# Optimization experiments

Measured on AMD Instinct MI355X. Metric: run time of the kernel, lower is better.

The kernel has to match this reference:

```python
import jax, jax.numpy as jnp
import numpy as np

N = 8192
IN_F = 256
OUT_F = 256
ATTN_DIM = 2
NEG_INF = -1e18


def setup_inputs() -> dict:
    key = jax.random.key(0)
    k1, k2, k3, k4, k5 = jax.random.split(key, 5)
    node_feats = jax.random.normal(k1, (N, IN_F), dtype=jnp.float32)
    Ahat = (jax.random.uniform(k2, (N, N)) < 0.01).astype(jnp.float32)
    # ensure no isolated rows (self loops) so softmax rows are well-defined
    Ahat = Ahat.at[jnp.arange(N), jnp.arange(N)].set(1.0)
    bound_w = 1.0 / np.sqrt(IN_F)
    bound_wa = 1.0 / np.sqrt(OUT_F)
    bound_a = 1.0 / np.sqrt(2 * ATTN_DIM)
    w = jax.random.uniform(k3, (IN_F, OUT_F), minval=-bound_w, maxval=bound_w, dtype=jnp.float32)
    w_a = jax.random.uniform(k4, (OUT_F, ATTN_DIM), minval=-bound_wa, maxval=bound_wa, dtype=jnp.float32)
    a = jax.random.uniform(k5, (2 * ATTN_DIM, 1), minval=-bound_a, maxval=bound_a, dtype=jnp.float32)
    return {"node_feats": node_feats, "Ahat": Ahat, "w": w, "w_a": w_a, "a": a}


def reference(node_feats, Ahat, w, w_a, a):
    # h_prime: [N, out_features]
    h_prime = node_feats @ w
    # h_reduced: [N, attn_dim]
    h_reduced = h_prime @ w_a
    # e[i, j] = cat(h_red[i], h_red[j]) @ a  ==  h_red[i]@a[:d] + h_red[j]@a[d:]
    # (identical math to the repeat+cat+matmul in the original, without the
    #  O(N^2 * 2d) materialization)
    f_src = (h_reduced @ a[:ATTN_DIM]).squeeze(-1)  # [N]
    f_dst = (h_reduced @ a[ATTN_DIM:]).squeeze(-1)  # [N]
    e = f_src[:, None] + f_dst[None, :]             # [N, N]
    masked_e = jnp.where(Ahat > 0, e, NEG_INF)
    attn_scores = jax.nn.softmax(masked_e, axis=-1)  # [N, N]
    out = attn_scores @ h_prime                      # [N, out_features]
    return jax.nn.relu(out)
```

## Files before the change

kernel.cpp:

```cpp
#include <hip/hip_runtime.h>
#include <hip/hip_bf16.h>
#include <math.h>

#define NN 8192
#define IN_F 256
#define OUT_F 256

typedef _Float16 half4_t __attribute__((ext_vector_type(4)));
typedef float    f4_t    __attribute__((ext_vector_type(4)));

#define KC 32
#define LS 68

__global__ __launch_bounds__(256) void gemm_hprime(
    const float* __restrict__ X,
    const float* __restrict__ W,
    _Float16* __restrict__ H16)
{
    __shared__ float As[KC * LS];
    __shared__ float Bs[KC * LS];

    const int tid  = threadIdx.x;
    const int row0 = blockIdx.x * 64;
    const int col0 = blockIdx.y * 64;
    const int tx   = tid & 15;
    const int ty   = tid >> 4;

    float acc[4][4];
#pragma unroll
    for (int i = 0; i < 4; ++i)
#pragma unroll
        for (int j = 0; j < 4; ++j) acc[i][j] = 0.0f;

    for (int k0 = 0; k0 < IN_F; k0 += KC) {
        {
            const int k4 = tid & 7;
            const int r0 = tid >> 3;
#pragma unroll
            for (int rp = 0; rp < 2; ++rp) {
                const int r = r0 + rp * 32;
                const float4 v = *(const float4*)(X + (size_t)(row0 + r) * IN_F + k0 + k4 * 4);
                As[(k4 * 4 + 0) * LS + r] = v.x;
                As[(k4 * 4 + 1) * LS + r] = v.y;
                As[(k4 * 4 + 2) * LS + r] = v.z;
                As[(k4 * 4 + 3) * LS + r] = v.w;
            }
        }
        {
            const int c4 = tid & 15;
            const int kb = tid >> 4;
#pragma unroll
            for (int kp = 0; kp < 2; ++kp) {
                const int k = kb + kp * 16;
                *(float4*)(&Bs[k * LS + c4 * 4]) =
                    *(const float4*)(W + (size_t)(k0 + k) * OUT_F + col0 + c4 * 4);
            }
        }
        __syncthreads();

#pragma unroll
        for (int k = 0; k < KC; ++k) {
            const float4 av = *(const float4*)(&As[k * LS + ty * 4]);
            const float4 bv = *(const float4*)(&Bs[k * LS + tx * 4]);
            const float a_[4] = {av.x, av.y, av.z, av.w};
            const float b_[4] = {bv.x, bv.y, bv.z, bv.w};
#pragma unroll
            for (int i = 0; i < 4; ++i)
#pragma unroll
                for (int j = 0; j < 4; ++j)
                    acc[i][j] = fmaf(a_[i], b_[j], acc[i][j]);
        }
        __syncthreads();
    }

#pragma unroll
    for (int i = 0; i < 4; ++i) {
        half4_t o;
        o.x = (_Float16)acc[i][0];
        o.y = (_Float16)acc[i][1];
        o.z = (_Float16)acc[i][2];
        o.w = (_Float16)acc[i][3];
        *(half4_t*)(H16 + (size_t)(row0 + ty * 4 + i) * OUT_F + col0 + tx * 4) = o;
    }
}

__global__ __launch_bounds__(256) void fdst_exp(
    const _Float16* __restrict__ hp16,
    const float* __restrict__ w_a,
    const float* __restrict__ a,
    float* __restrict__ fexp)
{
    const int row  = blockIdx.x * 4 + (threadIdx.x >> 6);
    const int lane = threadIdx.x & 63;

    const float a2 = a[2];
    const float a3 = a[3];

    const half4_t h  = ((const half4_t*)hp16)[(size_t)row * 64 + lane];
    const float4 wa0 = *(const float4*)(w_a + lane * 8);
    const float4 wa1 = *(const float4*)(w_a + lane * 8 + 4);

    float s = (float)h.x * fmaf(wa0.x, a2, wa0.y * a3)
            + (float)h.y * fmaf(wa0.z, a2, wa0.w * a3)
            + (float)h.z * fmaf(wa1.x, a2, wa1.y * a3)
            + (float)h.w * fmaf(wa1.z, a2, wa1.w * a3);

#pragma unroll
    for (int off = 32; off > 0; off >>= 1) s += __shfl_xor(s, off, 64);

    if (lane == 0) fexp[row] = expf(s);
}

#define CAPW 192

__global__ __launch_bounds__(256) void attn_aggregate(
    const float* __restrict__ Ahat,
    const _Float16* __restrict__ hp16,
    const float* __restrict__ fexp,
    float* __restrict__ out)
{
    __shared__ int s_idx[4 * CAPW];

    const int wid  = threadIdx.x >> 6;
    const int lane = threadIdx.x & 63;
    const int row  = blockIdx.x * 4 + wid;
    int* const my_idx = s_idx + wid * CAPW;

    const f4_t* arow   = (const f4_t*)(Ahat + (size_t)row * NN);
    const half4_t* hp4 = (const half4_t*)hp16;

    int cnt = 0;
    f4_t v0 = __builtin_nontemporal_load(arow + lane);
    f4_t v1 = __builtin_nontemporal_load(arow + 64 + lane);

    for (int c = 0; c < 32; ++c) {
        const f4_t cur = v0;
        v0 = v1;
        if (c + 2 < 32) v1 = __builtin_nontemporal_load(arow + (c + 2) * 64 + lane);

        const int jbase = c * 256 + lane * 4;

#define COMPACT(pred, comp)                                                   \
        {                                                                     \
            const unsigned long long m = __ballot(pred);                      \
            const unsigned int lo = __builtin_amdgcn_mbcnt_lo((unsigned)m, 0);\
            const int pos = cnt + (int)__builtin_amdgcn_mbcnt_hi(             \
                                        (unsigned)(m >> 32), lo);             \
            if ((pred) && pos < CAPW) my_idx[pos] = jbase + (comp);           \
            cnt += __builtin_popcountll(m);                                   \
        }

        COMPACT(cur.x > 0.0f, 0)
        COMPACT(cur.y > 0.0f, 1)
        COMPACT(cur.z > 0.0f, 2)
        COMPACT(cur.w > 0.0f, 3)
#undef COMPACT
    }
    if (cnt > CAPW) cnt = CAPW;

    float4 acc = {0.0f, 0.0f, 0.0f, 0.0f};
    float den = 0.0f;

    int k = 0;
    for (; k + 8 <= cnt; k += 8) {
        const int4 ja = *(const int4*)(my_idx + k);
        const int4 jb = *(const int4*)(my_idx + k + 4);

        const float p0 = fexp[ja.x], p1 = fexp[ja.y], p2 = fexp[ja.z], p3 = fexp[ja.w];
        const float p4 = fexp[jb.x], p5 = fexp[jb.y], p6 = fexp[jb.z], p7 = fexp[jb.w];

        const half4_t h0 = hp4[((size_t)ja.x << 6) + lane];
        const half4_t h1 = hp4[((size_t)ja.y << 6) + lane];
        const half4_t h2 = hp4[((size_t)ja.z << 6) + lane];
        const half4_t h3 = hp4[((size_t)ja.w << 6) + lane];
        const half4_t h4 = hp4[((size_t)jb.x << 6) + lane];
        const half4_t h5 = hp4[((size_t)jb.y << 6) + lane];
        const half4_t h6 = hp4[((size_t)jb.z << 6) + lane];
        const half4_t h7 = hp4[((size_t)jb.w << 6) + lane];

        acc.x = fmaf(p0, (float)h0.x, acc.x); acc.y = fmaf(p0, (float)h0.y, acc.y);
        acc.z = fmaf(p0, (float)h0.z, acc.z); acc.w = fmaf(p0, (float)h0.w, acc.w);
        acc.x = fmaf(p1, (float)h1.x, acc.x); acc.y = fmaf(p1, (float)h1.y, acc.y);
        acc.z = fmaf(p1, (float)h1.z, acc.z); acc.w = fmaf(p1, (float)h1.w, acc.w);
        acc.x = fmaf(p2, (float)h2.x, acc.x); acc.y = fmaf(p2, (float)h2.y, acc.y);
        acc.z = fmaf(p2, (float)h2.z, acc.z); acc.w = fmaf(p2, (float)h2.w, acc.w);
        acc.x = fmaf(p3, (float)h3.x, acc.x); acc.y = fmaf(p3, (float)h3.y, acc.y);
        acc.z = fmaf(p3, (float)h3.z, acc.z); acc.w = fmaf(p3, (float)h3.w, acc.w);
        acc.x = fmaf(p4, (float)h4.x, acc.x); acc.y = fmaf(p4, (float)h4.y, acc.y);
        acc.z = fmaf(p4, (float)h4.z, acc.z); acc.w = fmaf(p4, (float)h4.w, acc.w);
        acc.x = fmaf(p5, (float)h5.x, acc.x); acc.y = fmaf(p5, (float)h5.y, acc.y);
        acc.z = fmaf(p5, (float)h5.z, acc.z); acc.w = fmaf(p5, (float)h5.w, acc.w);
        acc.x = fmaf(p6, (float)h6.x, acc.x); acc.y = fmaf(p6, (float)h6.y, acc.y);
        acc.z = fmaf(p6, (float)h6.z, acc.z); acc.w = fmaf(p6, (float)h6.w, acc.w);
        acc.x = fmaf(p7, (float)h7.x, acc.x); acc.y = fmaf(p7, (float)h7.y, acc.y);
        acc.z = fmaf(p7, (float)h7.z, acc.z); acc.w = fmaf(p7, (float)h7.w, acc.w);

        den += ((p0 + p1) + (p2 + p3)) + ((p4 + p5) + (p6 + p7));
    }
    for (; k < cnt; ++k) {
        const int j = my_idx[k];
        const float p = fexp[j];
        const half4_t h = hp4[((size_t)j << 6) + lane];
        acc.x = fmaf(p, (float)h.x, acc.x);
        acc.y = fmaf(p, (float)h.y, acc.y);
        acc.z = fmaf(p, (float)h.z, acc.z);
        acc.w = fmaf(p, (float)h.w, acc.w);
        den += p;
    }

    const float inv = 1.0f / den;
    float4 o;
    o.x = fmaxf(acc.x * inv, 0.0f);
    o.y = fmaxf(acc.y * inv, 0.0f);
    o.z = fmaxf(acc.z * inv, 0.0f);
    o.w = fmaxf(acc.w * inv, 0.0f);
    *(float4*)(out + (size_t)row * OUT_F + lane * 4) = o;
}

extern "C" void kernel_launch(void* const* d_in, const int* in_sizes, int n_in,
                              void* d_out, int out_size, void* d_ws, size_t ws_size,
                              hipStream_t stream) {
    const float* node_feats = (const float*)d_in[0];
    const float* Ahat       = (const float*)d_in[1];
    const float* w          = (const float*)d_in[2];
    const float* w_a        = (const float*)d_in[3];
    const float* a          = (const float*)d_in[4];
    float* out = (float*)d_out;

    _Float16* hp16 = (_Float16*)d_ws;
    float* fexp = (float*)(hp16 + (size_t)NN * OUT_F);

    gemm_hprime<<<dim3(NN / 64, OUT_F / 64), 256, 0, stream>>>(node_feats, w, hp16);
    fdst_exp<<<dim3(NN / 4), 256, 0, stream>>>(hp16, w_a, a, fexp);
    attn_aggregate<<<dim3(NN / 4), 256, 0, stream>>>(Ahat, hp16, fexp, out);
}
```

Baseline: 386.7 us.

## Compute h_prime GEMM with split-bf16 MFMA instead of fp32 FMA

Replaces the fp32 shared-memory tiled GEMM with a matrix-core kernel that splits inputs into high and low bf16 parts and uses three MFMA products to approximate fp32 accuracy. A new prep kernel transposes W and splits it into hi/lo bf16 arrays in the workspace. The goal is to cut the time of the feature projection stage. In exchange it adds an extra kernel launch, reads X without shared-memory reuse, and slightly reduces accuracy by dropping the lo*lo term.

```diff
diff --git a/kernel.cpp b/kernel.cpp
--- a/kernel.cpp
+++ b/kernel.cpp
@@ -8,80 +8,108 @@
 
 typedef _Float16 half4_t __attribute__((ext_vector_type(4)));
 typedef float    f4_t    __attribute__((ext_vector_type(4)));
-
-#define KC 32
-#define LS 68
-
-__global__ __launch_bounds__(256) void gemm_hprime(
+typedef short    short8  __attribute__((ext_vector_type(8)));
+typedef float    f32x4   __attribute__((ext_vector_type(4)));
+typedef unsigned short us4 __attribute__((ext_vector_type(4)));
+
+__global__ __launch_bounds__(256) void prep_wt(
+    const float* __restrict__ W,
+    unsigned short* __restrict__ WtHi,
+    unsigned short* __restrict__ WtLo)
+{
+    __shared__ float Ls[64 * 68];
+    const int tid = threadIdx.x;
+    const int c0  = (blockIdx.x & 3) * 64;
+    const int k0  = (blockIdx.x >> 2) * 64;
+
+#pragma unroll
+    for (int rep = 0; rep < 4; ++rep) {
+        const int k  = (tid >> 4) + rep * 16;
+        const int c4 = tid & 15;
+        const float4 v = *(const float4*)(W + (size_t)(k0 + k) * OUT_F + c0 + c4 * 4);
+        Ls[(c4 * 4 + 0) * 68 + k] = v.x;
+        Ls[(c4 * 4 + 1) * 68 + k] = v.y;
+        Ls[(c4 * 4 + 2) * 68 + k] = v.z;
+        Ls[(c4 * 4 + 3) * 68 + k] = v.w;
+    }
+    __syncthreads();
+
+#pragma unroll
+    for (int rep = 0; rep < 4; ++rep) {
+        const int c  = (tid >> 4) + rep * 16;
+        const int k4 = tid & 15;
+        const float4 v = *(const float4*)(&Ls[c * 68 + k4 * 4]);
+        const float x[4] = {v.x, v.y, v.z, v.w};
+        us4 hi, lo;
+#pragma unroll
+        for (int j = 0; j < 4; ++j) {
+            const unsigned int bx = __float_as_uint(x[j]);
+            const unsigned int hb = bx & 0xFFFF0000u;
+            hi[j] = (unsigned short)(hb >> 16);
+            const float lf = x[j] - __uint_as_float(hb);
+            lo[j] = (unsigned short)(__float_as_uint(lf) >> 16);
+        }
+        const size_t off = (size_t)(c0 + c) * IN_F + k0 + k4 * 4;
+        *(us4*)(WtHi + off) = hi;
+        *(us4*)(WtLo + off) = lo;
+    }
+}
+
+__device__ __forceinline__ void split8(const float4 a, const float4 b,
+                                       short8& hi, short8& lo) {
+    const float x[8] = {a.x, a.y, a.z, a.w, b.x, b.y, b.z, b.w};
+#pragma unroll
+    for (int i = 0; i < 8; ++i) {
+        const unsigned int bx = __float_as_uint(x[i]);
+        const unsigned int hb = bx & 0xFFFF0000u;
+        hi[i] = (short)(hb >> 16);
+        const float lf = x[i] - __uint_as_float(hb);
+        lo[i] = (short)(__float_as_uint(lf) >> 16);
+    }
+}
+
+__global__ __launch_bounds__(256) void gemm_hprime_mfma(
     const float* __restrict__ X,
-    const float* __restrict__ W,
+    const unsigned short* __restrict__ WtHi,
+    const unsigned short* __restrict__ WtLo,
     _Float16* __restrict__ H16)
 {
-    __shared__ float As[KC * LS];
-    __shared__ float Bs[KC * LS];
-
-    const int tid  = threadIdx.x;
-    const int row0 = blockIdx.x * 64;
-    const int col0 = blockIdx.y * 64;
-    const int tx   = tid & 15;
-    const int ty   = tid >> 4;
-
-    float acc[4][4];
-#pragma unroll
-    for (int i = 0; i < 4; ++i)
-#pragma unroll
-        for (int j = 0; j < 4; ++j) acc[i][j] = 0.0f;
-
-    for (int k0 = 0; k0 < IN_F; k0 += KC) {
-        {
-            const int k4 = tid & 7;
-            const int r0 = tid >> 3;
-#pragma unroll
-            for (int rp = 0; rp < 2; ++rp) {
-                const int r = r0 + rp * 32;
-                const float4 v = *(const float4*)(X + (size_t)(row0 + r) * IN_F + k0 + k4 * 4);
-                As[(k4 * 4 + 0) * LS + r] = v.x;
-                As[(k4 * 4 + 1) * LS + r] = v.y;
-                As[(k4 * 4 + 2) * LS + r] = v.z;
-                As[(k4 * 4 + 3) * LS + r] = v.w;
-            }
+    const int w    = threadIdx.x >> 6;
+    const int lane = threadIdx.x & 63;
+    const int c0   = blockIdx.x * 64;
+    const int rw0  = blockIdx.y * 64 + w * 16;
+
+    const int ar = lane & 15;
+    const int ko = lane >> 4;
+
+    f32x4 acc[4] = {};
+
+    const float* xrow = X + (size_t)(rw0 + ar) * IN_F;
+
+    for (int k0 = 0; k0 < IN_F; k0 += 32) {
+        const float4 xa = *(const float4*)(xrow + k0 + ko * 8);
+        const float4 xb = *(const float4*)(xrow + k0 + ko * 8 + 4);
+        short8 ahi, alo;
+        split8(xa, xb, ahi, alo);
+
+#pragma unroll
+        for (int nc = 0; nc < 4; ++nc) {
+            const size_t boff = (size_t)(c0 + nc * 16 + ar) * IN_F + k0 + ko * 8;
+            const short8 bhi = *(const short8*)(WtHi + boff);
+            const short8 blo = *(const short8*)(WtLo + boff);
+            acc[nc] = __builtin_amdgcn_mfma_f32_16x16x32_bf16(ahi, bhi, acc[nc], 0, 0, 0);
+            acc[nc] = __builtin_amdgcn_mfma_f32_16x16x32_bf16(ahi, blo, acc[nc], 0, 0, 0);
+            acc[nc] = __builtin_amdgcn_mfma_f32_16x16x32_bf16(alo, bhi, acc[nc], 0, 0, 0);
         }
-        {
-            const int c4 = tid & 15;
-            const int kb = tid >> 4;
-#pragma unroll
-            for (int kp = 0; kp < 2; ++kp) {
-                const int k = kb + kp * 16;
-                *(float4*)(&Bs[k * LS + c4 * 4]) =
-                    *(const float4*)(W + (size_t)(k0 + k) * OUT_F + col0 + c4 * 4);
-            }
-        }
-        __syncthreads();
-
-#pragma unroll
-        for (int k = 0; k < KC; ++k) {
-            const float4 av = *(const float4*)(&As[k * LS + ty * 4]);
-            const float4 bv = *(const float4*)(&Bs[k * LS + tx * 4]);
-            const float a_[4] = {av.x, av.y, av.z, av.w};
-            const float b_[4] = {bv.x, bv.y, bv.z, bv.w};
-#pragma unroll
-            for (int i = 0; i < 4; ++i)
-#pragma unroll
-                for (int j = 0; j < 4; ++j)
-                    acc[i][j] = fmaf(a_[i], b_[j], acc[i][j]);
-        }
-        __syncthreads();
-    }
-
-#pragma unroll
-    for (int i = 0; i < 4; ++i) {
-        half4_t o;
-        o.x = (_Float16)acc[i][0];
-        o.y = (_Float16)acc[i][1];
-        o.z = (_Float16)acc[i][2];
-        o.w = (_Float16)acc[i][3];
-        *(half4_t*)(H16 + (size_t)(row0 + ty * 4 + i) * OUT_F + col0 + tx * 4) = o;
-    }
+    }
+
+    const int orow = rw0 + (lane >> 4) * 4;
+    const int ocol = c0 + (lane & 15);
+#pragma unroll
+    for (int nc = 0; nc < 4; ++nc)
+#pragma unroll
+        for (int i = 0; i < 4; ++i)
+            H16[(size_t)(orow + i) * OUT_F + ocol + nc * 16] = (_Float16)acc[nc][i];
 }
 
 __global__ __launch_bounds__(256) void fdst_exp(
@@ -228,9 +256,12 @@
     float* out = (float*)d_out;
 
     _Float16* hp16 = (_Float16*)d_ws;
-    float* fexp = (float*)(hp16 + (size_t)NN * OUT_F);
-
-    gemm_hprime<<<dim3(NN / 64, OUT_F / 64), 256, 0, stream>>>(node_feats, w, hp16);
+    float* fexp = (float*)((char*)d_ws + (size_t)NN * OUT_F * 2);
+    unsigned short* WtHi = (unsigned short*)((char*)fexp + NN * 4);
+    unsigned short* WtLo = WtHi + IN_F * OUT_F;
+
+    prep_wt<<<16, 256, 0, stream>>>(w, WtHi, WtLo);
+    gemm_hprime_mfma<<<dim3(OUT_F / 64, NN / 64), 256, 0, stream>>>(node_feats, WtHi, WtLo, hp16);
     fdst_exp<<<dim3(NN / 4), 256, 0, stream>>>(hp16, w_a, a, fexp);
     attn_aggregate<<<dim3(NN / 4), 256, 0, stream>>>(Ahat, hp16, fexp, out);
 }
```

Result: slower. 395.4 us (+2.3%).
